# Kernel optimization log

Hardware: AMD Instinct MI355X
Metric: run time of the kernel (lower is better)

## Reference

```python
import jax, jax.numpy as jnp
import numpy as np

B, T, C, H = 2, 2048, 1024, 16
D = C // H  # head_dim = 64

def setup_inputs() -> dict:
    key = jax.random.key(0)
    k1, k2, k3, k4, k5 = jax.random.split(key, 5)
    x = jax.random.normal(k1, (B, T, C), dtype=jnp.float32)
    # RoPE tables (realistic frequencies)
    inv_freq = 1.0 / (10000.0 ** (jnp.arange(0, D // 2, dtype=jnp.float32) / (D // 2)))
    pos = jnp.arange(T, dtype=jnp.float32)
    ang = pos[:, None] * inv_freq[None, :]          # (T, D/2)
    cos, sin = jnp.cos(ang), jnp.sin(ang)
    # causal mask (True = keep)
    mask = jnp.tril(jnp.ones((T, T), dtype=bool))
    W_qkv = jax.random.normal(k2, (3 * C, C), dtype=jnp.float32) * (1.0 / np.sqrt(C))
    W_out = jax.random.normal(k3, (C, C), dtype=jnp.float32) * (1.0 / np.sqrt(C))
    return {"x": x, "cos": cos, "sin": sin, "mask": mask, "W_qkv": W_qkv, "W_out": W_out}

def apply_rope(x, cos, sin):
    # x: (B, H, T, D); cos/sin: (T, D/2)
    d = x.shape[-1] // 2
    x1, x2 = x[..., :d], x[..., d:]
    c = cos[None, None, :x.shape[2], :]
    s = sin[None, None, :x.shape[2], :]
    return jnp.concatenate([x1 * c - x2 * s, x2 * c + x1 * s], axis=-1)

def reference(x, cos, sin, mask, W_qkv, W_out):
    b, t, c = x.shape
    qkv = (x @ W_qkv.T).reshape(b, t, 3, H, D)
    q, k, v = qkv[:, :, 0], qkv[:, :, 1], qkv[:, :, 2]   # (b, t, H, D)
    q = q.transpose(0, 2, 1, 3)
    k = k.transpose(0, 2, 1, 3)
    v = v.transpose(0, 2, 1, 3)                           # (b, H, t, D)
    q = apply_rope(q, cos, sin)
    k = apply_rope(k, cos, sin)
    attn = jnp.einsum('bhqd,bhkd->bhqk', q, k) / jnp.sqrt(jnp.asarray(D, x.dtype))
    attn = jnp.where(mask[None, None, :, :], attn, -jnp.inf)
    attn = jax.nn.softmax(attn, axis=-1)
    out = jnp.einsum('bhqk,bhkd->bhqd', attn, v)          # (b, H, t, D)
    out = out.transpose(0, 2, 1, 3).reshape(b, t, c)
    return out @ W_out.T
```

## Files before the change

### kernel.cpp

```cpp
#include <hip/hip_runtime.h>
#include <stdint.h>

typedef __bf16 bf16;
typedef __bf16 bf16x4 __attribute__((ext_vector_type(4)));
typedef __bf16 bf16x8 __attribute__((ext_vector_type(8)));
typedef float f32x4 __attribute__((ext_vector_type(4)));

#define TSEQ 2048
#define NHEAD 16
#define HDIM 64
#define CDIM 1024

#define AS1(p) ((const __attribute__((address_space(1))) void*)(p))
#define AS3(p) ((__attribute__((address_space(3))) void*)(p))

#if __has_builtin(__builtin_amdgcn_exp2f)
#define EXP2(x) __builtin_amdgcn_exp2f(x)
#else
#define EXP2(x) exp2f(x)
#endif

__global__ __launch_bounds__(256) void cast_bf16(const float* __restrict__ in,
                                                 bf16* __restrict__ out, int n) {
  int i = (blockIdx.x * 256 + threadIdx.x) * 8;
  if (i >= n) return;
  float4 a = *(const float4*)(in + i);
  float4 b = *(const float4*)(in + i + 4);
  bf16x8 r;
  r[0] = (bf16)a.x; r[1] = (bf16)a.y; r[2] = (bf16)a.z; r[3] = (bf16)a.w;
  r[4] = (bf16)b.x; r[5] = (bf16)b.y; r[6] = (bf16)b.z; r[7] = (bf16)b.w;
  *(bf16x8*)(out + i) = r;
}

__global__ __launch_bounds__(256) void cast2_bf16(const float* __restrict__ in1, int n1,
                                                  const float* __restrict__ in2, int n2,
                                                  bf16* __restrict__ out1,
                                                  bf16* __restrict__ out2) {
  int i = (blockIdx.x * 256 + threadIdx.x) * 8;
  const float* src;
  bf16* dst;
  if (i < n1) {
    src = in1 + i; dst = out1 + i;
  } else if (i < n1 + n2) {
    src = in2 + (i - n1); dst = out2 + (i - n1);
  } else {
    return;
  }
  float4 a = *(const float4*)src;
  float4 b = *(const float4*)(src + 4);
  bf16x8 r;
  r[0] = (bf16)a.x; r[1] = (bf16)a.y; r[2] = (bf16)a.z; r[3] = (bf16)a.w;
  r[4] = (bf16)b.x; r[5] = (bf16)b.y; r[6] = (bf16)b.z; r[7] = (bf16)b.w;
  *(bf16x8*)dst = r;
}

__global__ __launch_bounds__(256) void gemm_qkv_rope(const bf16* __restrict__ A,
                                                     const bf16* __restrict__ B,
                                                     const float* __restrict__ cosb,
                                                     const float* __restrict__ sinb,
                                                     bf16* __restrict__ Qb,
                                                     bf16* __restrict__ Kb,
                                                     bf16* __restrict__ Vraw) {
  constexpr int K = 1024;
  __shared__ bf16 As[128 * 32];
  __shared__ bf16 Bs[128 * 32];
  const int t = threadIdx.x;
  const int w = t >> 6, l = t & 63, g = l >> 4, ln = l & 15;
  const int wm = (w >> 1) * 64, wn = (w & 1) * 64;
  const int m0 = blockIdx.x * 128, n0 = blockIdx.y * 128;
  const int r0 = t >> 2, kc0 = (t & 3) * 8;

  f32x4 acc[4][4] = {};

  for (int k0 = 0; k0 < K; k0 += 32) {
    __syncthreads();
    __builtin_amdgcn_global_load_lds(AS1(A + (size_t)(m0 + r0) * K + k0 + kc0),
                                     AS3(&As[t * 8]), 16, 0, 0);
    __builtin_amdgcn_global_load_lds(AS1(A + (size_t)(m0 + r0 + 64) * K + k0 + kc0),
                                     AS3(&As[(t + 256) * 8]), 16, 0, 0);
    __builtin_amdgcn_global_load_lds(AS1(B + (size_t)(n0 + r0) * K + k0 + kc0),
                                     AS3(&Bs[t * 8]), 16, 0, 0);
    __builtin_amdgcn_global_load_lds(AS1(B + (size_t)(n0 + r0 + 64) * K + k0 + kc0),
                                     AS3(&Bs[(t + 256) * 8]), 16, 0, 0);
    __syncthreads();
    bf16x8 af[4], bfr[4];
#pragma unroll
    for (int i = 0; i < 4; i++) {
      af[i] = *(const bf16x8*)&As[(wm + i * 16 + ln) * 32 + g * 8];
      bfr[i] = *(const bf16x8*)&Bs[(wn + i * 16 + ln) * 32 + g * 8];
    }
#pragma unroll
    for (int i = 0; i < 4; i++)
#pragma unroll
      for (int j = 0; j < 4; j++)
        acc[i][j] = __builtin_amdgcn_mfma_f32_16x16x32_bf16(af[i], bfr[j], acc[i][j], 0, 0, 0);
  }

  const int part = n0 >> 10;
  if (part < 2) {
    bf16* dst = part ? Kb : Qb;
    const float qs = part ? 1.0f : 0.18033688011112042f;
#pragma unroll
    for (int i = 0; i < 4; i++)
#pragma unroll
      for (int j = 0; j < 2; j++) {
        int nl = (n0 & 1023) + wn + j * 16 + ln;
        int h = nl >> 6, d = nl & 31;
#pragma unroll
        for (int r = 0; r < 4; r++) {
          int row = m0 + wm + i * 16 + g * 4 + r;
          int tok = row & (TSEQ - 1), bb = row >> 11;
          float c = cosb[tok * 32 + d], s = sinb[tok * 32 + d];
          float a1 = acc[i][j][r], a2 = acc[i][j + 2][r];
          size_t ob = ((size_t)(bb * NHEAD + h) * TSEQ + tok) * HDIM + d;
          dst[ob] = (bf16)((a1 * c - a2 * s) * qs);
          dst[ob + 32] = (bf16)((a2 * c + a1 * s) * qs);
        }
      }
  } else {
#pragma unroll
    for (int i = 0; i < 4; i++)
#pragma unroll
      for (int j = 0; j < 4; j++) {
        int nl = (n0 & 1023) + wn + j * 16 + ln;
#pragma unroll
        for (int r = 0; r < 4; r++) {
          int row = m0 + wm + i * 16 + g * 4 + r;
          Vraw[(size_t)row * 1024 + nl] = (bf16)acc[i][j][r];
        }
      }
  }
}

__global__ __launch_bounds__(256) void gemm_out(const bf16* __restrict__ A,
                                                const bf16* __restrict__ B,
                                                float* __restrict__ C,
                                                int M, int N, int K) {
  __shared__ bf16 As[64 * 32];
  __shared__ bf16 Bs[128 * 32];
  const int t = threadIdx.x;
  const int w = t >> 6, l = t & 63, g = l >> 4, ln = l & 15;
  const int m0 = blockIdx.x * 64, n0 = blockIdx.y * 128;
  const int r0 = t >> 2, kc0 = (t & 3) * 8;

  f32x4 acc[4][2] = {};

  for (int k0 = 0; k0 < K; k0 += 32) {
    __syncthreads();
    __builtin_amdgcn_global_load_lds(AS1(A + (size_t)(m0 + r0) * K + k0 + kc0),
                                     AS3(&As[t * 8]), 16, 0, 0);
    __builtin_amdgcn_global_load_lds(AS1(B + (size_t)(n0 + r0) * K + k0 + kc0),
                                     AS3(&Bs[t * 8]), 16, 0, 0);
    __builtin_amdgcn_global_load_lds(AS1(B + (size_t)(n0 + r0 + 64) * K + k0 + kc0),
                                     AS3(&Bs[(t + 256) * 8]), 16, 0, 0);
    __syncthreads();
    bf16x8 af[4], bfr[2];
#pragma unroll
    for (int i = 0; i < 4; i++)
      af[i] = *(const bf16x8*)&As[(i * 16 + ln) * 32 + g * 8];
#pragma unroll
    for (int j = 0; j < 2; j++)
      bfr[j] = *(const bf16x8*)&Bs[(w * 32 + j * 16 + ln) * 32 + g * 8];
#pragma unroll
    for (int i = 0; i < 4; i++)
#pragma unroll
      for (int j = 0; j < 2; j++)
        acc[i][j] = __builtin_amdgcn_mfma_f32_16x16x32_bf16(af[i], bfr[j], acc[i][j], 0, 0, 0);
  }
#pragma unroll
  for (int i = 0; i < 4; i++)
#pragma unroll
    for (int j = 0; j < 2; j++) {
      int row = m0 + i * 16 + g * 4;
      int col = n0 + w * 32 + j * 16 + ln;
#pragma unroll
      for (int r = 0; r < 4; r++)
        C[(size_t)(row + r) * N + col] = acc[i][j][r];
    }
}

__global__ __launch_bounds__(256) void transpose_v(const bf16* __restrict__ Vraw,
                                                   bf16* __restrict__ Vt) {
  __shared__ bf16 Vs[64 * 72];
  const int t = threadIdx.x;
  const int tt = blockIdx.x;
  const int bh = blockIdx.y;
  const int b = bh >> 4, h = bh & (NHEAD - 1);
  for (int c = t; c < 512; c += 256) {
    int row = c >> 3, ch = c & 7;
    bf16x8 v = *(const bf16x8*)(Vraw + (size_t)(b * TSEQ + tt * 64 + row) * 1024 +
                                h * HDIM + ch * 8);
    *(bf16x8*)&Vs[row * 72 + ch * 8] = v;
  }
  __syncthreads();
  for (int c = t; c < 512; c += 256) {
    int d = c >> 3, ch = c & 7;
    bf16x8 o;
#pragma unroll
    for (int j = 0; j < 8; j++) o[j] = Vs[(ch * 8 + j) * 72 + d];
    *(bf16x8*)(Vt + ((size_t)(bh * HDIM + d)) * TSEQ + tt * 64 + ch * 8) = o;
  }
}

__global__ __launch_bounds__(512) void attn_fwd(const bf16* __restrict__ Q,
                                                const bf16* __restrict__ K,
                                                const bf16* __restrict__ Vt,
                                                bf16* __restrict__ ctx) {
  __shared__ bf16 Ks[2][64 * 72];
  __shared__ bf16 VTs[2][64 * 72];
  __shared__ bf16 Ps[8][16 * 72];
  __shared__ float Mrg[4][64][16];
  __shared__ float lred[4][16];
  __shared__ float linv[4][16];

  const int t = threadIdx.x;
  const int gp = t >> 8;
  const int tl = t & 255;
  const int w = t >> 6;
  const int w2 = w & 3;
  const int l = t & 63, g = l >> 4, ln = l & 15;
  const int bid = blockIdx.x;
  const int bh = bid & 31, pr = bid >> 5;
  const size_t base = (size_t)bh * TSEQ * HDIM;

  const int r0 = tl >> 3, r1 = (tl + 256) >> 3, ch0 = (tl & 7) * 8;
  bf16x8 kr0, kr1, vr0, vr1;

  for (int half = 0; half < 2; half++) {
    const int qb = half ? (31 - pr) : pr;
    const int q0 = qb * 64;
    const int q_global = q0 + w2 * 16 + ln;
    bf16x8 bq[2];
    bq[0] = *(const bf16x8*)(Q + base + (size_t)q_global * HDIM + g * 8);
    bq[1] = *(const bf16x8*)(Q + base + (size_t)q_global * HDIM + 32 + g * 8);
    f32x4 acc[4] = {};
    float l_run = 0.f;
    const int nit = (qb >> 1) + 1;

    if (gp <= qb) {
      kr0 = *(const bf16x8*)(K + base + (size_t)(gp * 64 + r0) * HDIM + ch0);
      kr1 = *(const bf16x8*)(K + base + (size_t)(gp * 64 + r1) * HDIM + ch0);
      vr0 = *(const bf16x8*)(Vt + base + (size_t)r0 * TSEQ + gp * 64 + ch0);
      vr1 = *(const bf16x8*)(Vt + base + (size_t)r1 * TSEQ + gp * 64 + ch0);
    }

    for (int i = 0; i < nit; i++) {
      const int kt = 2 * i + gp;
      const bool active = (kt <= qb);
      __syncthreads();
      if (active) {
        *(bf16x8*)&Ks[gp][r0 * 72 + ch0] = kr0;
        *(bf16x8*)&Ks[gp][r1 * 72 + ch0] = kr1;
        *(bf16x8*)&VTs[gp][r0 * 72 + ch0] = vr0;
        *(bf16x8*)&VTs[gp][r1 * 72 + ch0] = vr1;
      }
      __syncthreads();
      const int ktn = kt + 2;
      if (ktn <= qb) {
        kr0 = *(const bf16x8*)(K + base + (size_t)(ktn * 64 + r0) * HDIM + ch0);
        kr1 = *(const bf16x8*)(K + base + (size_t)(ktn * 64 + r1) * HDIM + ch0);
        vr0 = *(const bf16x8*)(Vt + base + (size_t)r0 * TSEQ + ktn * 64 + ch0);
        vr1 = *(const bf16x8*)(Vt + base + (size_t)r1 * TSEQ + ktn * 64 + ch0);
      }
      if (active) {
        f32x4 st[4] = {};
#pragma unroll
        for (int step = 0; step < 2; step++)
#pragma unroll
          for (int mt = 0; mt < 4; mt++) {
            bf16x8 ak = *(const bf16x8*)&Ks[gp][(mt * 16 + ln) * 72 + step * 32 + g * 8];
            st[mt] = __builtin_amdgcn_mfma_f32_16x16x32_bf16(ak, bq[step], st[mt], 0, 0, 0);
          }
        float vals[16];
        if (kt == qb) {
#pragma unroll
          for (int mt = 0; mt < 4; mt++)
#pragma unroll
            for (int r = 0; r < 4; r++) {
              int kg = kt * 64 + mt * 16 + g * 4 + r;
              vals[mt * 4 + r] = (kg <= q_global) ? fminf(st[mt][r], 60.f) : -INFINITY;
            }
        } else {
#pragma unroll
          for (int mt = 0; mt < 4; mt++)
#pragma unroll
            for (int r = 0; r < 4; r++) vals[mt * 4 + r] = fminf(st[mt][r], 60.f);
        }
        float psum = 0.f;
#pragma unroll
        for (int i2 = 0; i2 < 16; i2++) {
          float p = EXP2(vals[i2]);
          vals[i2] = p;
          psum += p;
        }
        psum += __shfl_xor(psum, 16);
        psum += __shfl_xor(psum, 32);
        l_run += psum;
#pragma unroll
        for (int mt = 0; mt < 4; mt++) {
          bf16x4 pk;
#pragma unroll
          for (int r = 0; r < 4; r++) pk[r] = (bf16)vals[mt * 4 + r];
          *(bf16x4*)&Ps[w][ln * 72 + mt * 16 + g * 4] = pk;
        }
#pragma unroll
        for (int step = 0; step < 2; step++) {
          bf16x8 ap = *(const bf16x8*)&Ps[w][ln * 72 + step * 32 + g * 8];
#pragma unroll
          for (int nt = 0; nt < 4; nt++) {
            bf16x8 bv = *(const bf16x8*)&VTs[gp][(nt * 16 + ln) * 72 + step * 32 + g * 8];
            acc[nt] = __builtin_amdgcn_mfma_f32_16x16x32_bf16(ap, bv, acc[nt], 0, 0, 0);
          }
        }
      }
    }
    __syncthreads();
    if (gp == 1) {
#pragma unroll
      for (int nt = 0; nt < 4; nt++) *(f32x4*)&Mrg[w2][l][nt * 4] = acc[nt];
      if (l < 16) lred[w2][ln] = l_run;
    }
    __syncthreads();
    if (gp == 0) {
#pragma unroll
      for (int nt = 0; nt < 4; nt++) acc[nt] += *(const f32x4*)&Mrg[w2][l][nt * 4];
      float ltot = l_run + lred[w2][ln];
      if (l < 16) linv[w2][ln] = 1.0f / ltot;
      float lrow[4];
#pragma unroll
      for (int r = 0; r < 4; r++) lrow[r] = linv[w2][g * 4 + r];
      const int b = bh >> 4, h = bh & (NHEAD - 1);
#pragma unroll
      for (int nt = 0; nt < 4; nt++)
#pragma unroll
        for (int r = 0; r < 4; r++) {
          int q = q0 + w2 * 16 + g * 4 + r;
          ctx[(size_t)(b * TSEQ + q) * CDIM + h * HDIM + nt * 16 + ln] =
              (bf16)(acc[nt][r] * lrow[r]);
        }
    }
  }
}

extern "C" void kernel_launch(void* const* d_in, const int* in_sizes, int n_in,
                              void* d_out, int out_size, void* d_ws, size_t ws_size,
                              hipStream_t stream) {
  const float* x = (const float*)d_in[0];
  const float* cosb = (const float*)d_in[1];
  const float* sinb = (const float*)d_in[2];
  const float* Wqkv = (const float*)d_in[4];
  const float* Wout = (const float*)d_in[5];
  float* out = (float*)d_out;

  char* ws = (char*)d_ws;
  bf16* x_bf = (bf16*)ws;
  bf16* ctx = (bf16*)ws;
  bf16* Wqkv_bf = (bf16*)(ws + 8388608);
  bf16* Wout_bf = (bf16*)(ws + 8388608);
  bf16* Qb = (bf16*)(ws + 14680064);
  bf16* Kb = (bf16*)(ws + 23068672);
  bf16* Vraw = (bf16*)(ws + 31457280);
  bf16* Vt = (bf16*)(ws + 39845888);

  cast2_bf16<<<(4194304 + 3145728) / 8 / 256, 256, 0, stream>>>(
      x, 4194304, Wqkv, 3145728, x_bf, Wqkv_bf);
  gemm_qkv_rope<<<dim3(32, 24), 256, 0, stream>>>(x_bf, Wqkv_bf, cosb, sinb, Qb, Kb, Vraw);
  cast_bf16<<<1048576 / 8 / 256, 256, 0, stream>>>(Wout, Wout_bf, 1048576);
  transpose_v<<<dim3(32, 32), 256, 0, stream>>>(Vraw, Vt);
  attn_fwd<<<512, 512, 0, stream>>>(Qb, Kb, Vt, ctx);
  gemm_out<<<dim3(64, 8), 256, 0, stream>>>(ctx, Wout_bf, out, 4096, 1024, 1024);
}
```

Measured before the change: 195.1 us.

## Fuse V transpose into QKV GEMM epilogue and merge weight casts

After: 188.7 us. 1.03x faster.

```diff
diff --git a/kernel.cpp b/kernel.cpp
--- a/kernel.cpp
+++ b/kernel.cpp
@@ -20,22 +20,12 @@
 #define EXP2(x) exp2f(x)
 #endif
 
-__global__ __launch_bounds__(256) void cast_bf16(const float* __restrict__ in,
-                                                 bf16* __restrict__ out, int n) {
-  int i = (blockIdx.x * 256 + threadIdx.x) * 8;
-  if (i >= n) return;
-  float4 a = *(const float4*)(in + i);
-  float4 b = *(const float4*)(in + i + 4);
-  bf16x8 r;
-  r[0] = (bf16)a.x; r[1] = (bf16)a.y; r[2] = (bf16)a.z; r[3] = (bf16)a.w;
-  r[4] = (bf16)b.x; r[5] = (bf16)b.y; r[6] = (bf16)b.z; r[7] = (bf16)b.w;
-  *(bf16x8*)(out + i) = r;
-}
-
-__global__ __launch_bounds__(256) void cast2_bf16(const float* __restrict__ in1, int n1,
+__global__ __launch_bounds__(256) void cast3_bf16(const float* __restrict__ in1, int n1,
                                                   const float* __restrict__ in2, int n2,
+                                                  const float* __restrict__ in3, int n3,
                                                   bf16* __restrict__ out1,
-                                                  bf16* __restrict__ out2) {
+                                                  bf16* __restrict__ out2,
+                                                  bf16* __restrict__ out3) {
   int i = (blockIdx.x * 256 + threadIdx.x) * 8;
   const float* src;
   bf16* dst;
@@ -43,6 +33,8 @@
     src = in1 + i; dst = out1 + i;
   } else if (i < n1 + n2) {
     src = in2 + (i - n1); dst = out2 + (i - n1);
+  } else if (i < n1 + n2 + n3) {
+    src = in3 + (i - n1 - n2); dst = out3 + (i - n1 - n2);
   } else {
     return;
   }
@@ -60,10 +52,9 @@
                                                      const float* __restrict__ sinb,
                                                      bf16* __restrict__ Qb,
                                                      bf16* __restrict__ Kb,
-                                                     bf16* __restrict__ Vraw) {
+                                                     bf16* __restrict__ Vt) {
   constexpr int K = 1024;
-  __shared__ bf16 As[128 * 32];
-  __shared__ bf16 Bs[128 * 32];
+  __shared__ bf16 smem[8704];
   const int t = threadIdx.x;
   const int w = t >> 6, l = t & 63, g = l >> 4, ln = l & 15;
   const int wm = (w >> 1) * 64, wn = (w & 1) * 64;
@@ -75,19 +66,19 @@
   for (int k0 = 0; k0 < K; k0 += 32) {
     __syncthreads();
     __builtin_amdgcn_global_load_lds(AS1(A + (size_t)(m0 + r0) * K + k0 + kc0),
-                                     AS3(&As[t * 8]), 16, 0, 0);
+                                     AS3(&smem[t * 8]), 16, 0, 0);
     __builtin_amdgcn_global_load_lds(AS1(A + (size_t)(m0 + r0 + 64) * K + k0 + kc0),
-                                     AS3(&As[(t + 256) * 8]), 16, 0, 0);
+                                     AS3(&smem[(t + 256) * 8]), 16, 0, 0);
     __builtin_amdgcn_global_load_lds(AS1(B + (size_t)(n0 + r0) * K + k0 + kc0),
-                                     AS3(&Bs[t * 8]), 16, 0, 0);
+                                     AS3(&smem[4096 + t * 8]), 16, 0, 0);
     __builtin_amdgcn_global_load_lds(AS1(B + (size_t)(n0 + r0 + 64) * K + k0 + kc0),
-                                     AS3(&Bs[(t + 256) * 8]), 16, 0, 0);
+                                     AS3(&smem[4096 + (t + 256) * 8]), 16, 0, 0);
     __syncthreads();
     bf16x8 af[4], bfr[4];
 #pragma unroll
     for (int i = 0; i < 4; i++) {
-      af[i] = *(const bf16x8*)&As[(wm + i * 16 + ln) * 32 + g * 8];
-      bfr[i] = *(const bf16x8*)&Bs[(wn + i * 16 + ln) * 32 + g * 8];
+      af[i] = *(const bf16x8*)&smem[(wm + i * 16 + ln) * 32 + g * 8];
+      bfr[i] = *(const bf16x8*)&smem[4096 + (wn + i * 16 + ln) * 32 + g * 8];
     }
 #pragma unroll
     for (int i = 0; i < 4; i++)
@@ -118,17 +109,36 @@
         }
       }
   } else {
-#pragma unroll
-    for (int i = 0; i < 4; i++)
-#pragma unroll
-      for (int j = 0; j < 4; j++) {
-        int nl = (n0 & 1023) + wn + j * 16 + ln;
-#pragma unroll
-        for (int r = 0; r < 4; r++) {
-          int row = m0 + wm + i * 16 + g * 4 + r;
-          Vraw[(size_t)row * 1024 + nl] = (bf16)acc[i][j][r];
-        }
-      }
+    const int bb = m0 >> 11;
+    const int tbase = m0 & (TSEQ - 1);
+    const int nbase = n0 - 2048;
+#pragma unroll
+    for (int pass = 0; pass < 2; pass++) {
+      __syncthreads();
+      if ((w >> 1) == pass) {
+#pragma unroll
+        for (int i = 0; i < 4; i++)
+#pragma unroll
+          for (int j = 0; j < 4; j++) {
+            int lr = i * 16 + g * 4;
+            int lc = wn + j * 16 + ln;
+#pragma unroll
+            for (int r = 0; r < 4; r++)
+              smem[(lr + r) * 132 + lc] = (bf16)acc[i][j][r];
+          }
+      }
+      __syncthreads();
+      for (int c = t; c < 1024; c += 256) {
+        int ch = c >> 3, tc = c & 7;
+        bf16x8 o;
+#pragma unroll
+        for (int j2 = 0; j2 < 8; j2++) o[j2] = smem[(tc * 8 + j2) * 132 + ch];
+        int n = nbase + ch;
+        int h = n >> 6, d = n & 63;
+        *(bf16x8*)(Vt + ((size_t)((bb * NHEAD + h) * HDIM + d)) * TSEQ +
+                   tbase + pass * 64 + tc * 8) = o;
+      }
+    }
   }
 }
 
@@ -179,29 +189,6 @@
     }
 }
 
-__global__ __launch_bounds__(256) void transpose_v(const bf16* __restrict__ Vraw,
-                                                   bf16* __restrict__ Vt) {
-  __shared__ bf16 Vs[64 * 72];
-  const int t = threadIdx.x;
-  const int tt = blockIdx.x;
-  const int bh = blockIdx.y;
-  const int b = bh >> 4, h = bh & (NHEAD - 1);
-  for (int c = t; c < 512; c += 256) {
-    int row = c >> 3, ch = c & 7;
-    bf16x8 v = *(const bf16x8*)(Vraw + (size_t)(b * TSEQ + tt * 64 + row) * 1024 +
-                                h * HDIM + ch * 8);
-    *(bf16x8*)&Vs[row * 72 + ch * 8] = v;
-  }
-  __syncthreads();
-  for (int c = t; c < 512; c += 256) {
-    int d = c >> 3, ch = c & 7;
-    bf16x8 o;
-#pragma unroll
-    for (int j = 0; j < 8; j++) o[j] = Vs[(ch * 8 + j) * 72 + d];
-    *(bf16x8*)(Vt + ((size_t)(bh * HDIM + d)) * TSEQ + tt * 64 + ch * 8) = o;
-  }
-}
-
 __global__ __launch_bounds__(512) void attn_fwd(const bf16* __restrict__ Q,
                                                 const bf16* __restrict__ K,
                                                 const bf16* __restrict__ Vt,
@@ -356,17 +343,14 @@
   bf16* x_bf = (bf16*)ws;
   bf16* ctx = (bf16*)ws;
   bf16* Wqkv_bf = (bf16*)(ws + 8388608);
-  bf16* Wout_bf = (bf16*)(ws + 8388608);
-  bf16* Qb = (bf16*)(ws + 14680064);
-  bf16* Kb = (bf16*)(ws + 23068672);
-  bf16* Vraw = (bf16*)(ws + 31457280);
-  bf16* Vt = (bf16*)(ws + 39845888);
-
-  cast2_bf16<<<(4194304 + 3145728) / 8 / 256, 256, 0, stream>>>(
-      x, 4194304, Wqkv, 3145728, x_bf, Wqkv_bf);
-  gemm_qkv_rope<<<dim3(32, 24), 256, 0, stream>>>(x_bf, Wqkv_bf, cosb, sinb, Qb, Kb, Vraw);
-  cast_bf16<<<1048576 / 8 / 256, 256, 0, stream>>>(Wout, Wout_bf, 1048576);
-  transpose_v<<<dim3(32, 32), 256, 0, stream>>>(Vraw, Vt);
+  bf16* Wout_bf = (bf16*)(ws + 14680064);
+  bf16* Qb = (bf16*)(ws + 16777216);
+  bf16* Kb = (bf16*)(ws + 25165824);
+  bf16* Vt = (bf16*)(ws + 33554432);
+
+  cast3_bf16<<<(4194304 + 3145728 + 1048576) / 8 / 256, 256, 0, stream>>>(
+      x, 4194304, Wqkv, 3145728, Wout, 1048576, x_bf, Wqkv_bf, Wout_bf);
+  gemm_qkv_rope<<<dim3(32, 24), 256, 0, stream>>>(x_bf, Wqkv_bf, cosb, sinb, Qb, Kb, Vt);
   attn_fwd<<<512, 512, 0, stream>>>(Qb, Kb, Vt, ctx);
   gemm_out<<<dim3(64, 8), 256, 0, stream>>>(ctx, Wout_bf, out, 4096, 1024, 1024);
 }
```
